# Kernel tuning notes

Measured on AMD Instinct MI355X. Metric: run time of the kernel, lower is better.

## Reference

```python
import jax, jax.numpy as jnp
import numpy as np

# Grid / modeling constants (match init_kwargs)
NX, NY = 512, 512
NT = 400
ORDER = 8
NE = ORDER // 2          # halo width
H = 10.0                 # grid spacing (m)
DT = 0.001               # time step (s)
DIMX = NX + ORDER
DIMY = NY + ORDER
# 8th-order second-derivative FD coefficients
C0, C1, C2, C3, C4 = -205.0 / 72.0, 8.0 / 5.0, -1.0 / 5.0, 8.0 / 315.0, -1.0 / 560.0
_COEF = (C1, C2, C3, C4)


def setup_inputs() -> dict:
    key = jax.random.key(0)
    k1, k2 = jax.random.split(key)
    # realistic acoustic velocity model, 1500-2500 m/s
    vel = 1500.0 + 1000.0 * jax.random.uniform(k1, (NX, NY), dtype=jnp.float32)
    w = jax.random.normal(k2, (NT,), dtype=jnp.float32)  # source wavelet
    return {"vel": vel, "w": w, "sx": 256, "sy": 4, "ry": 4}


def _laplacian(u):
    # order-8 cross stencil in x and y (grid is (dimy, dimx), x fast)
    l = 2.0 * C0 * u
    for k, c in zip((1, 2, 3, 4), _COEF):
        l = l + c * (jnp.roll(u, k, 0) + jnp.roll(u, -k, 0)
                     + jnp.roll(u, k, 1) + jnp.roll(u, -k, 1))
    return l


def _forward(vel, w, sx, sy, ry):
    # vel: (nx, ny) y-fast -> vpad: (dimy, dimx) x-fast, replication padded
    vpad = jnp.pad(vel.T, NE, mode="edge")
    scale = (vpad * DT) ** 2 / (H * H)          # (v*dt/h)^2 per cell
    mask = jnp.zeros((DIMY, DIMX), vel.dtype).at[NE:NE + NY, NE:NE + NX].set(1.0)
    iy, ix = sy + NE, sx + NE
    src_amp = (vpad[iy, ix] * DT) ** 2           # dt^2 * v^2 at source

    def step(carry, wt):
        u1, u2 = carry
        lap = _laplacian(u2)
        u3 = (2.0 * u2 - u1 + scale * lap) * mask  # zero Dirichlet halo
        u3 = u3.at[iy, ix].add(wt * src_amp)       # source injection
        rec = u3[ry + NE, NE:NE + NX]              # record x-line at depth ry
        return (u2, u3), rec

    u0 = jnp.zeros((DIMY, DIMX), vel.dtype)
    _, frd = jax.lax.scan(jax.checkpoint(step), (u0, u0), w)
    return frd  # (nt, nx)


def reference(vel, w, sx, sy, ry):
    return _forward(vel, w, sx, sy, ry)
```

## Files before the change

### kernel.cpp

```cpp
#include <hip/hip_runtime.h>

typedef float f32x4 __attribute__((ext_vector_type(4)));

#define NXg   512
#define NYg   512
#define NTt   400
#define DIMg  520
#define DTc   0.001f
#define Hc    10.0f
#define KSTEP 4
#define NCHUNK (NTt / KSTEP)

#define C0f (-205.0f/72.0f)
#define C1f (8.0f/5.0f)
#define C2f (-1.0f/5.0f)
#define C3f (8.0f/315.0f)
#define C4f (-1.0f/560.0f)

__global__ void time2d_init(const float* __restrict__ vel,
                            float* __restrict__ scale,
                            float* __restrict__ fields ) {
    int idx = blockIdx.x * blockDim.x + threadIdx.x;
    if (idx < DIMg * DIMg) {
        int y = idx / DIMg;
        int x = idx - y * DIMg;
        float s = 0.0f;
        if (y >= 4 && y < 516 && x >= 4 && x < 516) {
            float v = vel[(x - 4) * NYg + (y - 4)] * DTc;
            s = v * v / (Hc * Hc);
        }
        scale[idx] = s;
    }
    for (int i = idx; i < 4 * DIMg * DIMg; i += gridDim.x * blockDim.x)
        fields[i] = 0.0f;
}

__launch_bounds__(256)
__global__ void time2d_chunk(const float* __restrict__ Ps,
                             const float* __restrict__ Cs,
                             float* __restrict__ Pd,
                             float* __restrict__ Cd,
                             const float* __restrict__ scale,
                             const float* __restrict__ w,
                             const float* __restrict__ vel,
                             const int* __restrict__ sxp,
                             const int* __restrict__ syp,
                             const int* __restrict__ ryp,
                             float* __restrict__ out,
                             int t0)
{
    const int tid = threadIdx.x;
    const int bx  = blockIdx.x, by = blockIdx.y;

    const int sx = *sxp, sy = *syp, ry = *ryp;
    const int iy = sy + 4, ix = sx + 4, iyr = ry + 4;
    const float va  = vel[sx * NYg + sy] * DTc;
    const float amp = va * va;

    const int xc = tid & 15, yg = tid >> 4;
    const int x4 = xc * 4, rb = yg * 4;
    const bool active = (yg < 14);
    const int lx0 = bx * 32 - 12, ly0 = by * 32 - 12;
    const int gx0 = lx0 + x4;
    const bool ownedCol = (x4 >= 16 && x4 < 48);

    f32x4 scq[4];
    int srcI = -1, srcJ = 0;
    bool rec[4]; int gyv[4];
    #pragma unroll
    for (int i = 0; i < 4; ++i) {
        const int gy = ly0 + 4 + rb + i;
        gyv[i] = gy;
        f32x4 s = (f32x4)0.0f;
        if ((unsigned)gy < 520u && (unsigned)gx0 < 517u)
            s = *(const f32x4*)&scale[gy * DIMg + gx0];
        scq[i] = s;
        #pragma unroll
        for (int j = 0; j < 4; ++j)
            if (gy == iy && gx0 + j == ix) { srcI = i; srcJ = j; }
        rec[i] = (gy == iyr) && ownedCol && ((unsigned)(rb + i - 12) < 32u);
    }

    __shared__ float lds[2][64 * 64];

    #pragma unroll
    for (int ii = 0; ii < 4; ++ii) {
        const int pos = (tid + 256 * ii) * 4;
        const int ty = pos >> 6, tx = pos & 63;
        const int gy = ly0 + ty, gx = lx0 + tx;
        f32x4 v = (f32x4)0.0f;
        if ((unsigned)gy < 520u && (unsigned)gx < 520u)
            v = *(const f32x4*)&Cs[gy * DIMg + gx];
        *(f32x4*)&lds[0][pos] = v;
    }
    f32x4 prevq[4], valq[4];
    #pragma unroll
    for (int i = 0; i < 4; ++i) {
        const int gy = gyv[i];
        f32x4 v = (f32x4)0.0f;
        if ((unsigned)gy < 520u && (unsigned)gx0 < 520u)
            v = *(const f32x4*)&Ps[gy * DIMg + gx0];
        prevq[i] = v;
    }
    __syncthreads();

    int p = 0;
    #pragma unroll
    for (int k = 0; k < KSTEP; ++k) {
        const int t = t0 + k;
        const float inj = (srcI >= 0) ? w[t] * amp : 0.0f;
        const float* cur = lds[p];
        float* nxt = lds[p ^ 1];
        if (active) {
            f32x4 win[12];
            #pragma unroll
            for (int m = 0; m < 12; ++m)
                win[m] = *(const f32x4*)&cur[(rb + m) * 64 + x4];
            #pragma unroll
            for (int i = 0; i < 4; ++i) {
                const int y = 4 + rb + i;
                const f32x4 lq = *(const f32x4*)&cur[y * 64 + x4 - 4];
                const f32x4 rq = *(const f32x4*)&cur[y * 64 + x4 + 4];
                float h[12];
                #pragma unroll
                for (int j = 0; j < 4; ++j) {
                    h[j] = lq[j]; h[4 + j] = win[4 + i][j]; h[8 + j] = rq[j];
                }
                f32x4 nv;
                #pragma unroll
                for (int j = 0; j < 4; ++j) {
                    const float ctr = h[4 + j];
                    const float lap = 2.0f * C0f * ctr
                      + C1f * (win[3 + i][j] + win[5 + i][j] + h[3 + j] + h[5 + j])
                      + C2f * (win[2 + i][j] + win[6 + i][j] + h[2 + j] + h[6 + j])
                      + C3f * (win[1 + i][j] + win[7 + i][j] + h[1 + j] + h[7 + j])
                      + C4f * (win[0 + i][j] + win[8 + i][j] + h[0 + j] + h[8 + j]);
                    float nvj = 2.0f * ctr - prevq[i][j] + scq[i][j] * lap;
                    if (srcI == i && srcJ == j) nvj += inj;
                    nv[j] = nvj;
                    prevq[i][j] = ctr;
                }
                *(f32x4*)&nxt[y * 64 + x4] = nv;
                valq[i] = nv;
                if (rec[i])
                    *(f32x4*)&out[(size_t)t * NXg + (gx0 - 4)] = nv;
            }
        }
        __syncthreads();
        p ^= 1;
    }

    if (ownedCol) {
        #pragma unroll
        for (int i = 0; i < 4; ++i) {
            if ((unsigned)(rb + i - 12) < 32u) {
                const size_t g = (size_t)gyv[i] * DIMg + gx0;
                *(f32x4*)&Pd[g] = prevq[i];
                *(f32x4*)&Cd[g] = valq[i];
            }
        }
    }
}

extern "C" void kernel_launch(void* const* d_in, const int* in_sizes, int n_in,
                              void* d_out, int out_size, void* d_ws, size_t ws_size,
                              hipStream_t stream) {
    const float* vel = (const float*)d_in[0];
    const float* w   = (const float*)d_in[1];
    const int*   sx  = (const int*)d_in[2];
    const int*   sy  = (const int*)d_in[3];
    const int*   ry  = (const int*)d_in[4];
    float* out = (float*)d_out;

    float* ws    = (float*)d_ws;
    float* scale = ws;
    float* fld   = ws + DIMg * DIMg;
    float* P[2]  = { fld,                fld + 2 * DIMg * DIMg };
    float* C[2]  = { fld + DIMg * DIMg,  fld + 3 * DIMg * DIMg };

    time2d_init<<<(DIMg * DIMg + 255) / 256, 256, 0, stream>>>(vel, scale, fld);

    dim3 grid(16, 16);
    for (int c = 0; c < NCHUNK; ++c) {
        const int s = c & 1, d = s ^ 1;
        time2d_chunk<<<grid, 256, 0, stream>>>(P[s], C[s], P[d], C[d],
                                               scale, w, vel, sx, sy, ry,
                                               out, c * KSTEP);
    }
}
```

Before: 932.5 us.

## Widen temporal-blocking halo to 80x80 tiles, six steps per launch

Time steps fused per launch go from 4 to 6. The shared tile grows from 64x64 to 80x84 with a 20-cell halo, and blocks now have 512 threads. This cuts the launch count from 100 to 67 and reduces global-memory round trips of the wavefields. Source amplitudes are precomputed into a params buffer by the init kernel, so the chunk kernel no longer reads vel, w or the scalar inputs each launch. The cost is more redundant halo computation per block (80x80 computed for a 32x32 owned region) and higher LDS and register pressure.

```diff
diff --git a/kernel.cpp b/kernel.cpp
--- a/kernel.cpp
+++ b/kernel.cpp
@@ -8,8 +8,11 @@
 #define DIMg  520
 #define DTc   0.001f
 #define Hc    10.0f
-#define KSTEP 4
-#define NCHUNK (NTt / KSTEP)
+
+#define TILE   80
+#define TSTR   84
+#define NQROW  20
+#define NQUADS (TILE*NQROW)
 
 #define C0f (-205.0f/72.0f)
 #define C1f (8.0f/5.0f)
@@ -18,8 +21,13 @@
 #define C4f (-1.0f/560.0f)
 
 __global__ void time2d_init(const float* __restrict__ vel,
+                            const float* __restrict__ w,
+                            const int* __restrict__ sxp,
+                            const int* __restrict__ syp,
+                            const int* __restrict__ ryp,
                             float* __restrict__ scale,
-                            float* __restrict__ fields ) {
+                            float* __restrict__ fields,
+                            float* __restrict__ params) {
     int idx = blockIdx.x * blockDim.x + threadIdx.x;
     if (idx < DIMg * DIMg) {
         int y = idx / DIMg;
@@ -33,94 +41,101 @@
     }
     for (int i = idx; i < 4 * DIMg * DIMg; i += gridDim.x * blockDim.x)
         fields[i] = 0.0f;
+    if (idx < NTt) {
+        const int sx = *sxp, sy = *syp;
+        const float va = vel[sx * NYg + sy] * DTc;
+        params[4 + idx] = w[idx] * (va * va);
+    }
+    if (idx == 0) {
+        int* pi = (int*)params;
+        pi[0] = *syp + 4;
+        pi[1] = *sxp + 4;
+        pi[2] = *ryp + 4;
+    }
 }
 
-__launch_bounds__(256)
+template<int K>
+__launch_bounds__(512)
 __global__ void time2d_chunk(const float* __restrict__ Ps,
                              const float* __restrict__ Cs,
                              float* __restrict__ Pd,
                              float* __restrict__ Cd,
                              const float* __restrict__ scale,
-                             const float* __restrict__ w,
-                             const float* __restrict__ vel,
-                             const int* __restrict__ sxp,
-                             const int* __restrict__ syp,
-                             const int* __restrict__ ryp,
+                             const float* __restrict__ params,
                              float* __restrict__ out,
                              int t0)
 {
     const int tid = threadIdx.x;
-    const int bx  = blockIdx.x, by = blockIdx.y;
-
-    const int sx = *sxp, sy = *syp, ry = *ryp;
-    const int iy = sy + 4, ix = sx + 4, iyr = ry + 4;
-    const float va  = vel[sx * NYg + sy] * DTc;
-    const float amp = va * va;
-
-    const int xc = tid & 15, yg = tid >> 4;
-    const int x4 = xc * 4, rb = yg * 4;
-    const bool active = (yg < 14);
-    const int lx0 = bx * 32 - 12, ly0 = by * 32 - 12;
+    const int bx = blockIdx.x, by = blockIdx.y;
+    const int lx0 = bx * 32 - 20, ly0 = by * 32 - 20;
+
+    const int* pi = (const int*)params;
+    const int srcY = pi[0], srcX = pi[1], recY = pi[2];
+
+    __shared__ float lds[2][TILE * TSTR];
+
+    #pragma unroll
+    for (int ii = 0; ii < 4; ++ii) {
+        const int pos = tid + 512 * ii;
+        if (pos < NQUADS) {
+            const int ty = pos / NQROW, txq = pos - ty * NQROW;
+            const int gy = ly0 + ty, gx = lx0 + txq * 4;
+            f32x4 v = (f32x4)0.0f;
+            if ((unsigned)gy < 520u && (unsigned)gx < 517u)
+                v = *(const f32x4*)&Cs[gy * DIMg + gx];
+            *(f32x4*)&lds[0][ty * TSTR + txq * 4] = v;
+        }
+    }
+
+    const int ct = tid;
+    const bool active = (ct < 360);
+    const int xc = ct % NQROW, yg = ct / NQROW;
+    const int x4 = xc * 4;
+    const int rb = 4 + yg * 4;
     const int gx0 = lx0 + x4;
-    const bool ownedCol = (x4 >= 16 && x4 < 48);
-
-    f32x4 scq[4];
+    const bool ownedCol = (xc >= 6 && xc < 14);
+    const bool ownedRow = ((unsigned)(rb - 24) < 32u);
+
+    f32x4 scq[4], prevq[4], valq[4];
     int srcI = -1, srcJ = 0;
-    bool rec[4]; int gyv[4];
+    bool rec[4];
     #pragma unroll
     for (int i = 0; i < 4; ++i) {
-        const int gy = ly0 + 4 + rb + i;
-        gyv[i] = gy;
-        f32x4 s = (f32x4)0.0f;
-        if ((unsigned)gy < 520u && (unsigned)gx0 < 517u)
-            s = *(const f32x4*)&scale[gy * DIMg + gx0];
-        scq[i] = s;
+        const int gy = ly0 + rb + i;
+        f32x4 s = (f32x4)0.0f, pv = (f32x4)0.0f;
+        if (active && (unsigned)gy < 520u && (unsigned)gx0 < 517u) {
+            s  = *(const f32x4*)&scale[gy * DIMg + gx0];
+            pv = *(const f32x4*)&Ps[gy * DIMg + gx0];
+        }
+        scq[i] = s; prevq[i] = pv;
         #pragma unroll
         for (int j = 0; j < 4; ++j)
-            if (gy == iy && gx0 + j == ix) { srcI = i; srcJ = j; }
-        rec[i] = (gy == iyr) && ownedCol && ((unsigned)(rb + i - 12) < 32u);
-    }
-
-    __shared__ float lds[2][64 * 64];
-
-    #pragma unroll
-    for (int ii = 0; ii < 4; ++ii) {
-        const int pos = (tid + 256 * ii) * 4;
-        const int ty = pos >> 6, tx = pos & 63;
-        const int gy = ly0 + ty, gx = lx0 + tx;
-        f32x4 v = (f32x4)0.0f;
-        if ((unsigned)gy < 520u && (unsigned)gx < 520u)
-            v = *(const f32x4*)&Cs[gy * DIMg + gx];
-        *(f32x4*)&lds[0][pos] = v;
-    }
-    f32x4 prevq[4], valq[4];
-    #pragma unroll
-    for (int i = 0; i < 4; ++i) {
-        const int gy = gyv[i];
-        f32x4 v = (f32x4)0.0f;
-        if ((unsigned)gy < 520u && (unsigned)gx0 < 520u)
-            v = *(const f32x4*)&Ps[gy * DIMg + gx0];
-        prevq[i] = v;
-    }
+            if (gy == srcY && gx0 + j == srcX) { srcI = i; srcJ = j; }
+        rec[i] = active && ownedCol && ownedRow && (gy == recY);
+    }
+
+    float injs[K];
+    #pragma unroll
+    for (int k = 0; k < K; ++k)
+        injs[k] = (srcI >= 0) ? params[4 + t0 + k] : 0.0f;
+
     __syncthreads();
 
     int p = 0;
     #pragma unroll
-    for (int k = 0; k < KSTEP; ++k) {
-        const int t = t0 + k;
-        const float inj = (srcI >= 0) ? w[t] * amp : 0.0f;
+    for (int k = 0; k < K; ++k) {
         const float* cur = lds[p];
         float* nxt = lds[p ^ 1];
         if (active) {
             f32x4 win[12];
             #pragma unroll
             for (int m = 0; m < 12; ++m)
-                win[m] = *(const f32x4*)&cur[(rb + m) * 64 + x4];
+                win[m] = *(const f32x4*)&cur[(rb - 4 + m) * TSTR + x4];
             #pragma unroll
             for (int i = 0; i < 4; ++i) {
-                const int y = 4 + rb + i;
-                const f32x4 lq = *(const f32x4*)&cur[y * 64 + x4 - 4];
-                const f32x4 rq = *(const f32x4*)&cur[y * 64 + x4 + 4];
+                const int y = rb + i;
+                const f32x4 lq = *(const f32x4*)&cur[y * TSTR + x4 - 4];
+                const f32x4 rq = *(const f32x4*)&cur[y * TSTR + x4 + 4];
                 float h[12];
                 #pragma unroll
                 for (int j = 0; j < 4; ++j) {
@@ -136,28 +151,26 @@
                       + C3f * (win[1 + i][j] + win[7 + i][j] + h[1 + j] + h[7 + j])
                       + C4f * (win[0 + i][j] + win[8 + i][j] + h[0 + j] + h[8 + j]);
                     float nvj = 2.0f * ctr - prevq[i][j] + scq[i][j] * lap;
-                    if (srcI == i && srcJ == j) nvj += inj;
+                    if (srcI == i && srcJ == j) nvj += injs[k];
                     nv[j] = nvj;
                     prevq[i][j] = ctr;
                 }
-                *(f32x4*)&nxt[y * 64 + x4] = nv;
+                *(f32x4*)&nxt[y * TSTR + x4] = nv;
                 valq[i] = nv;
                 if (rec[i])
-                    *(f32x4*)&out[(size_t)t * NXg + (gx0 - 4)] = nv;
+                    *(f32x4*)&out[(size_t)(t0 + k) * NXg + (gx0 - 4)] = nv;
             }
         }
         __syncthreads();
         p ^= 1;
     }
 
-    if (ownedCol) {
+    if (active && ownedCol && ownedRow) {
         #pragma unroll
         for (int i = 0; i < 4; ++i) {
-            if ((unsigned)(rb + i - 12) < 32u) {
-                const size_t g = (size_t)gyv[i] * DIMg + gx0;
-                *(f32x4*)&Pd[g] = prevq[i];
-                *(f32x4*)&Cd[g] = valq[i];
-            }
+            const size_t g = (size_t)(ly0 + rb + i) * DIMg + gx0;
+            *(f32x4*)&Pd[g] = prevq[i];
+            *(f32x4*)&Cd[g] = valq[i];
         }
     }
 }
@@ -172,19 +185,25 @@
     const int*   ry  = (const int*)d_in[4];
     float* out = (float*)d_out;
 
-    float* ws    = (float*)d_ws;
-    float* scale = ws;
-    float* fld   = ws + DIMg * DIMg;
-    float* P[2]  = { fld,                fld + 2 * DIMg * DIMg };
-    float* C[2]  = { fld + DIMg * DIMg,  fld + 3 * DIMg * DIMg };
-
-    time2d_init<<<(DIMg * DIMg + 255) / 256, 256, 0, stream>>>(vel, scale, fld);
+    float* ws     = (float*)d_ws;
+    float* scale  = ws;
+    float* params = ws + DIMg * DIMg;
+    float* fld    = params + 512;
+    float* P[2]   = { fld,               fld + 2 * DIMg * DIMg };
+    float* C[2]   = { fld + DIMg * DIMg, fld + 3 * DIMg * DIMg };
+
+    time2d_init<<<(DIMg * DIMg + 255) / 256, 256, 0, stream>>>(
+        vel, w, sx, sy, ry, scale, fld, params);
 
     dim3 grid(16, 16);
-    for (int c = 0; c < NCHUNK; ++c) {
+    for (int c = 0; c < 66; ++c) {
         const int s = c & 1, d = s ^ 1;
-        time2d_chunk<<<grid, 256, 0, stream>>>(P[s], C[s], P[d], C[d],
-                                               scale, w, vel, sx, sy, ry,
-                                               out, c * KSTEP);
+        time2d_chunk<6><<<grid, 512, 0, stream>>>(P[s], C[s], P[d], C[d],
+                                                  scale, params, out, c * 6);
+    }
+    {
+        const int c = 66, s = c & 1, d = s ^ 1;
+        time2d_chunk<4><<<grid, 512, 0, stream>>>(P[s], C[s], P[d], C[d],
+                                                  scale, params, out, 396);
     }
 }
```

Measured after the change: 880.9 us. 1.06x faster.
